# Kernel tuning notes

Hardware: AMD Instinct MI355X
Metric: run time of the kernel (lower is better)

The kernel has to match this reference:

```python
import jax, jax.numpy as jnp
import numpy as np
from jax import lax

D = 30   # embedding_dim (hardcoded in repo)
Q = 30   # question length
N = 4000 # number of sentences in doc
S = 100  # tokens per sentence
K = 5    # k_for_maxpool
SLOPE = 0.1  # LeakyReLU negative slope


def setup_inputs() -> dict:
    key = jax.random.key(0)
    ks = jax.random.split(key, 20)
    rn = lambda k, sh: jax.random.normal(k, sh, dtype=jnp.float32)
    ru = lambda k, sh: jax.random.uniform(k, sh, dtype=jnp.float32)
    return {
        "doc_sents_embeds": rn(ks[0], (N, S, D)),
        "sents_gaf": ru(ks[1], (N, 3)),
        "question_embeds": rn(ks[2], (Q, D)),
        "q_idfs": ru(ks[3], (Q, 1)),
        "doc_gaf": ru(ks[4], (4,)),
        "conv1_w": rn(ks[5], (D, D, 3)) * 0.1,
        "conv1_b": rn(ks[6], (D,)) * 0.1,
        "conv2_w": rn(ks[7], (D, D, 3)) * 0.1,
        "conv2_b": rn(ks[8], (D,)) * 0.1,
        "qw_W": rn(ks[9], (1, D + 1)) * 0.1,
        "qw_b": rn(ks[10], (1,)) * 0.1,
        "lq1_W": rn(ks[11], (8, 6)) * 0.1,
        "lq1_b": rn(ks[12], (8,)) * 0.1,
        "lq2_W": rn(ks[13], (1, 8)) * 0.1,
        "lq2_b": rn(ks[14], (1,)) * 0.1,
        "so_W": rn(ks[15], (1, 4)) * 0.1,
        "so_b": rn(ks[16], (1,)) * 0.1,
        "fl_W": rn(ks[17], (1, 5)) * 0.1,
        "fl_b": rn(ks[18], (1,)) * 0.1,
    }


def _leaky(x):
    return jnp.where(x >= 0, x, SLOPE * x)


def _conv_block(x, w, b):
    # x: [B, L, D]. torch Conv1d(D, D, 3, padding=2) then slice [1:L+1]
    # is exactly a 'same' conv with padding 1 on each side; then residual add.
    y = lax.conv_general_dilated(x.transpose(0, 2, 1), w, (1,), [(1, 1)],
                                 dimension_numbers=("NCH", "OIH", "NCH"))
    y = _leaky(y + b[None, :, None])
    return y.transpose(0, 2, 1) + x


def _cos_sim(A, B):
    # A: [Q, D], B: [N, S, D] -> [N, Q, S] (num/den as in torch my_cosine_sim)
    num = jnp.einsum("qd,nsd->nqs", A, B)
    den = jnp.linalg.norm(A, axis=-1)[None, :, None] * jnp.linalg.norm(B, axis=-1)[:, None, :]
    return num / den


def _pool(sim):
    # sort-based k-max pooling -> [max, avg_of_top_k]; sim: [N, Q, S] -> [N, Q, 2]
    vals = lax.top_k(sim, K)[0]  # descending
    return jnp.stack([vals[..., 0], vals.mean(-1)], axis=-1)


def reference(doc_sents_embeds, sents_gaf, question_embeds, q_idfs, doc_gaf,
              conv1_w, conv1_b, conv2_w, conv2_b, qw_W, qw_b,
              lq1_W, lq1_b, lq2_W, lq2_b, so_W, so_b, fl_W, fl_b):
    # question context (two residual trigram convs)
    q_conv = _conv_block(question_embeds[None], conv1_w, conv1_b)
    q_conv = _conv_block(q_conv, conv2_w, conv2_b)[0]          # [Q, D]
    # question term weights
    qw_in = jnp.concatenate([q_conv, q_idfs], axis=-1)          # [Q, D+1]
    q_weights = jax.nn.softmax((qw_in @ qw_W.T + qw_b)[:, 0])   # [Q]
    # sentence context convs (batched over all sentences)
    conv_res = _conv_block(doc_sents_embeds, conv1_w, conv1_b)
    conv_res = _conv_block(conv_res, conv2_w, conv2_b)          # [N, S, D]
    # similarity matrices
    sim_insens = _cos_sim(question_embeds, doc_sents_embeds)    # [N, Q, S]
    sim_oh = (sim_insens > 1.0 - 1e-3).astype(sim_insens.dtype)
    sim_sens = _cos_sim(q_conv, conv_res)
    # k-max pooling and per-q tiny MLP attention
    feats = jnp.concatenate([_pool(sim_oh), _pool(sim_insens), _pool(sim_sens)], axis=-1)  # [N, Q, 6]
    lo = _leaky(feats @ lq1_W.T + lq1_b) @ lq2_W.T + lq2_b      # [N, Q, 1]
    lo = lo[..., 0] * q_weights[None, :]
    sent_emit = lo.sum(-1) / Q                                  # [N]
    # per-sentence output layer
    sent_feats = jnp.concatenate([sents_gaf, sent_emit[:, None]], axis=-1)  # [N, 4]
    sent_scores = jax.nn.sigmoid((sent_feats @ so_W.T + so_b)[:, 0])        # [N]
    # doc-level score
    doc_rep = jnp.concatenate([jnp.max(sent_scores)[None], doc_gaf])        # [5]
    final = doc_rep @ fl_W.T + fl_b                                          # [1]
    return final, sent_scores
```

## Files before the change

### kernel.cpp

```cpp
#include <hip/hip_runtime.h>
#include <hip/hip_bf16.h>

#define SLOPE 0.1f

#define OFF_QW    1816
#define OFF_QNI   1846
#define OFF_QNS   1876
#define OFF_QNN   1906
#define OFF_B1    4606
#define OFF_B2    7336
#define OFF_LQ1W  7366
#define OFF_LQ1B  7414
#define OFF_LQ2W  7422
#define OFF_LQ2B  7430
#define OFF_SOW   7431
#define OFF_SOB   7435
#define OFF_FLW   7436
#define OFF_FLB   7441
#define U16_QEA   16384
#define U16_QCA   17408
#define U16_WB1   18432
#define U16_WB2   21504

typedef __attribute__((ext_vector_type(8))) __bf16 bf16x8;
typedef __attribute__((ext_vector_type(4))) float f32x4;

union Frag { uint4 u4; uint u[4]; bf16x8 v; };

__device__ __forceinline__ float bf2f(ushort h) {
    union { uint u; float f; } c; c.u = ((uint)h) << 16; return c.f;
}
__device__ __forceinline__ ushort f2bf(float f) {
    union { float f; uint u; } c; c.f = f;
    uint u = c.u;
    return (ushort)((u + 0x7FFFu + ((u >> 16) & 1u)) >> 16);
}
__device__ __forceinline__ float ldx(const void* p, long i, int bf) {
    if (bf) return bf2f(((const ushort*)p)[i]);
    return ((const float*)p)[i];
}
#define CE(x, y) { float _hi = fmaxf(x, y), _lo = fminf(x, y); x = _hi; y = _lo; }

__device__ __forceinline__ void sort4d(float& a, float& b, float& c, float& d) {
    CE(a, b); CE(c, d); CE(a, c); CE(b, d); CE(b, c);
}
__device__ __forceinline__ void merge44_5(const float* a, const float* b, float* t) {
    t[0] = fmaxf(a[0], b[0]);
    t[1] = fmaxf(fminf(a[0], b[0]), fmaxf(a[1], b[1]));
    t[2] = fmaxf(fmaxf(fminf(a[0], b[1]), fminf(a[1], b[0])), fmaxf(a[2], b[2]));
    t[3] = fmaxf(fmaxf(fminf(a[0], b[2]), fminf(a[1], b[1])),
                 fmaxf(fminf(a[2], b[0]), fmaxf(a[3], b[3])));
    t[4] = fmaxf(fmaxf(fminf(a[0], b[3]), fminf(a[1], b[2])),
                 fmaxf(fminf(a[2], b[1]), fminf(a[3], b[0])));
}
__device__ __forceinline__ void merge54_5(const float* a, const float* b, float* t) {
    t[0] = fmaxf(a[0], b[0]);
    t[1] = fmaxf(fminf(a[0], b[0]), fmaxf(a[1], b[1]));
    t[2] = fmaxf(fmaxf(fminf(a[0], b[1]), fminf(a[1], b[0])), fmaxf(a[2], b[2]));
    t[3] = fmaxf(fmaxf(fminf(a[0], b[2]), fminf(a[1], b[1])),
                 fmaxf(fminf(a[2], b[0]), fmaxf(a[3], b[3])));
    t[4] = fmaxf(fmaxf(fmaxf(fminf(a[0], b[3]), fminf(a[1], b[2])),
                       fmaxf(fminf(a[2], b[1]), fminf(a[3], b[0]))), a[4]);
}
__device__ __forceinline__ void merge55_5(const float* a, const float* b, float* t) {
    t[0] = fmaxf(a[0], b[0]);
    t[1] = fmaxf(fminf(a[0], b[0]), fmaxf(a[1], b[1]));
    t[2] = fmaxf(fmaxf(fminf(a[0], b[1]), fminf(a[1], b[0])), fmaxf(a[2], b[2]));
    t[3] = fmaxf(fmaxf(fminf(a[0], b[2]), fminf(a[1], b[1])),
                 fmaxf(fminf(a[2], b[0]), fmaxf(a[3], b[3])));
    t[4] = fmaxf(fmaxf(fmaxf(fminf(a[0], b[3]), fminf(a[1], b[2])),
                       fmaxf(fminf(a[2], b[1]), fminf(a[3], b[0]))),
                 fmaxf(a[4], b[4]));
}

__device__ __forceinline__ int detect_bf(const void* doc_in, int tid, int* scnt) {
    if (tid == 0) *scnt = 0;
    __syncthreads();
    const ushort* p = (const ushort*)doc_in;
    int local = 0;
    for (int i = tid; i < 4096; i += 256) {
        unsigned e = (p[i] >> 7) & 0xFFu;
        if (e != 0u && (e < 100u || e > 134u)) local++;
    }
    atomicAdd(scnt, local);
    __syncthreads();
    return (*scnt > 200) ? 0 : 1;
}

__global__ __launch_bounds__(256) void k_prep(
        const void* doc_in,
        const void* qe_in, const void* qidf_in,
        const void* w1_in, const void* b1_in,
        const void* w2_in, const void* b2_in,
        const void* qwW_in, const void* qwb_in,
        const void* lq1W_in, const void* lq1b_in,
        const void* lq2W_in, const void* lq2b_in,
        const void* soW_in, const void* sob_in,
        const void* flW_in, const void* flb_in,
        float* ws) {
    const int tid = threadIdx.x;
    const int blk = blockIdx.x;
    __shared__ float QE[900], T1[900], QC[900], W[2700], IDF[32], LG[32];
    __shared__ int scnt;

    const int bf = detect_bf(doc_in, tid, &scnt);
    ushort* wsu = (ushort*)ws;

    if (blk == 1) {
        if (tid == 0) { ((int*)ws)[0] = bf; }
        if (tid < 30) ws[OFF_B1 + tid] = ldx(b1_in, tid, bf);
        if (tid < 48) ws[OFF_LQ1W + tid] = ldx(lq1W_in, tid, bf);
        if (tid < 8)  { ws[OFF_LQ1B + tid] = ldx(lq1b_in, tid, bf);
                        ws[OFF_LQ2W + tid] = ldx(lq2W_in, tid, bf); }
        if (tid < 4)  ws[OFF_SOW + tid] = ldx(soW_in, tid, bf);
        if (tid < 5)  ws[OFF_FLW + tid] = ldx(flW_in, tid, bf);
        if (tid == 1) { ws[OFF_LQ2B] = ldx(lq2b_in, 0, bf);
                        ws[OFF_SOB]  = ldx(sob_in, 0, bf);
                        ws[OFF_FLB]  = ldx(flb_in, 0, bf); }
        for (int i = tid; i < 3072; i += 256) {
            int o = i / 96, kk = i % 96;
            float v1 = 0.f;
            if (o < 30 && kk < 90) {
                int ii = kk % 30, k = kk / 30;
                v1 = ldx(w1_in, (long)o*90 + ii*3 + k, bf);
            }
            wsu[U16_WB1 + i] = f2bf(v1);
        }
        return;
    }
    if (blk == 2) {
        if (tid < 30) ws[OFF_B2 + tid] = ldx(b2_in, tid, bf);
        for (int i = tid; i < 3072; i += 256) {
            int o = i / 96, kk = i % 96;
            float v2 = 0.f;
            if (o < 30 && kk < 90) {
                int ii = kk % 30, k = kk / 30;
                v2 = ldx(w2_in, (long)o*90 + ii*3 + k, bf);
            }
            wsu[U16_WB2 + i] = f2bf(v2);
        }
        return;
    }

    if (tid == 0) { ((int*)ws)[0] = bf; }

    for (int i = tid; i < 900; i += 256) QE[i] = ldx(qe_in, i, bf);
    if (tid < 30) IDF[tid] = ldx(qidf_in, tid, bf);
    for (int i = tid; i < 2700; i += 256) W[i] = ldx(w1_in, i, bf);
    __syncthreads();

    for (int idx = tid; idx < 900; idx += 256) {
        int s = idx / 30, o = idx % 30;
        float acc = ldx(b1_in, o, bf);
        for (int k = 0; k < 3; ++k) {
            int t = s + k - 1;
            if (t < 0 || t >= 30) continue;
            for (int i = 0; i < 30; ++i) acc += QE[t*30 + i] * W[o*90 + i*3 + k];
        }
        acc = acc >= 0.f ? acc : SLOPE * acc;
        T1[idx] = acc + QE[idx];
    }
    __syncthreads();
    for (int i = tid; i < 2700; i += 256) W[i] = ldx(w2_in, i, bf);
    __syncthreads();
    for (int idx = tid; idx < 900; idx += 256) {
        int s = idx / 30, o = idx % 30;
        float acc = ldx(b2_in, o, bf);
        for (int k = 0; k < 3; ++k) {
            int t = s + k - 1;
            if (t < 0 || t >= 30) continue;
            for (int i = 0; i < 30; ++i) acc += T1[t*30 + i] * W[o*90 + i*3 + k];
        }
        acc = acc >= 0.f ? acc : SLOPE * acc;
        QC[idx] = acc + T1[idx];
    }
    __syncthreads();

    if (tid < 30) {
        float s1 = 0.f, s2 = 0.f;
        for (int d = 0; d < 30; ++d) {
            float a = QE[tid*30 + d]; s1 += a*a;
            float b = QC[tid*30 + d]; s2 += b*b;
        }
        float n1 = sqrtf(s1);
        ws[OFF_QNN + tid] = n1;
        ws[OFF_QNI + tid] = 1.0f / n1;
        ws[OFF_QNS + tid] = 1.0f / sqrtf(s2);
        float z = ldx(qwb_in, 0, bf);
        for (int d = 0; d < 30; ++d) z += QC[tid*30 + d] * ldx(qwW_in, d, bf);
        z += IDF[tid] * ldx(qwW_in, 30, bf);
        LG[tid] = z;
    }
    __syncthreads();
    if (tid == 0) {
        float m = -1e30f;
        for (int q = 0; q < 30; ++q) m = fmaxf(m, LG[q]);
        float sum = 0.f, e[30];
        for (int q = 0; q < 30; ++q) { e[q] = expf(LG[q] - m); sum += e[q]; }
        for (int q = 0; q < 30; ++q) ws[OFF_QW + q] = e[q] / sum;
    }
    for (int i = tid; i < 1024; i += 256) {
        int q = i >> 5, d = i & 31;
        float ve = (q < 30 && d < 30) ? QE[q*30 + d] : 0.f;
        float vc = (q < 30 && d < 30) ? QC[q*30 + d] : 0.f;
        wsu[U16_QEA + i] = f2bf(ve);
        wsu[U16_QCA + i] = f2bf(vc);
    }
}

__global__ __launch_bounds__(128, 4) void k_main(const void* doc_in, const void* gaf_in,
                                                 void* out, float* ws) {
    const int n = blockIdx.x;
    const int tid = threadIdx.x;
    const int bf = ((const int*)ws)[0];
    const int lane = tid & 63;
    const int wid = tid >> 6;
    const int l15 = lane & 15;
    const int quad = lane >> 4;

    __shared__ uint XA32[1546];
    __shared__ uint XB32[1546];
    __shared__ __align__(16) float INVX[112];
    __shared__ float FE[30][6];
    __shared__ float IQI[32], IQS[32], QNN[32], BI1[32], BI2[32];

    ushort* XAu = (ushort*)XA32;
    const ushort* wsu = (const ushort*)ws;
    const uint4* qeA = (const uint4*)(wsu + U16_QEA);
    const uint4* qcA = (const uint4*)(wsu + U16_QCA);
    const uint4* wb1 = (const uint4*)(wsu + U16_WB1);
    const uint4* wb2 = (const uint4*)(wsu + U16_WB2);

    float ga0 = ldx(gaf_in, (long)n*3 + 0, bf);
    float ga1 = ldx(gaf_in, (long)n*3 + 1, bf);
    float ga2 = ldx(gaf_in, (long)n*3 + 2, bf);

    for (int i = tid; i < 46; i += 128) {
        int j = (i < 15) ? i : (1500 + i);
        XA32[j] = 0u; XB32[j] = 0u;
    }
    if (tid >= 100 && tid < 112) INVX[tid] = 0.f;
    if (bf) {
        const uint* g = (const uint*)((const ushort*)doc_in + (size_t)n * 3000);
        for (int i = tid; i < 1500; i += 128) XA32[15 + i] = g[i];
    } else {
        const float* p = (const float*)doc_in + (size_t)n * 3000;
        for (int i = tid; i < 3000; i += 128) XAu[30 + i] = f2bf(p[i]);
    }
    if (tid < 32) {
        IQI[tid] = ws[OFF_QNI + tid];
        IQS[tid] = ws[OFF_QNS + tid];
        QNN[tid] = ws[OFF_QNN + tid];
        BI1[tid] = ws[OFF_B1 + tid];
        BI2[tid] = ws[OFF_B2 + tid];
    }
    __syncthreads();

    if (tid < 100) {
        const uint* r = XA32 + (tid + 1) * 15;
        float s = 0.f;
        #pragma unroll
        for (int i = 0; i < 15; ++i) {
            uint u = r[i];
            float lo = __uint_as_float(u << 16);
            float hi = __uint_as_float(u & 0xFFFF0000u);
            s += lo * lo + hi * hi;
        }
        INVX[tid] = 1.f / sqrtf(s);
    }
    __syncthreads();

    auto sim_pool = [&](const uint4* qa, const float* IQ, int fbase, bool do_oh) {
        const int q = wid * 16 + l15;
        Frag b;
        b.u4 = qa[q * 4 + quad];
        f32x4 acc[7];
        #pragma unroll
        for (int mt = 0; mt < 7; ++mt) {
            int m = mt * 16 + l15;
            Frag a;
            if (m < 100) {
                int base = (m + 1) * 15 + quad * 4;
                a.u[0] = XA32[base];     a.u[1] = XA32[base + 1];
                a.u[2] = XA32[base + 2]; a.u[3] = XA32[base + 3];
            } else { a.u[0] = a.u[1] = a.u[2] = a.u[3] = 0u; }
            f32x4 z = {0.f, 0.f, 0.f, 0.f};
            acc[mt] = __builtin_amdgcn_mfma_f32_16x16x32_bf16(a.v, b.v, z, 0, 0, 0);
        }
        const float4* INVX4 = (const float4*)INVX;
        float thr = 0.999f * QNN[q];
        float iq  = (q < 30) ? IQ[q] : 0.f;
        float g[7][4];
        int cnt = 0;
        #pragma unroll
        for (int mt = 0; mt < 7; ++mt) {
            float4 ix = INVX4[mt * 4 + quad];
            float ixa[4] = {ix.x, ix.y, ix.z, ix.w};
            #pragma unroll
            for (int r = 0; r < 4; ++r) {
                float u = acc[mt][r] * ixa[r];
                if (mt == 6 && (quad * 4 + r) >= 4) u = -1e30f;
                g[mt][r] = u;
                if (do_oh) cnt += (u > thr) ? 1 : 0;
            }
        }
        #pragma unroll
        for (int mt = 0; mt < 7; ++mt) sort4d(g[mt][0], g[mt][1], g[mt][2], g[mt][3]);
        float p0[5], p1[5], p2[5], q0[5], q1[5], t[5];
        merge44_5(g[0], g[1], p0);
        merge44_5(g[2], g[3], p1);
        merge44_5(g[4], g[5], p2);
        merge55_5(p0, p1, q0);
        merge54_5(p2, g[6], q1);
        merge55_5(q0, q1, t);
        #pragma unroll
        for (int d = 16; d < 64; d <<= 1) {
            float pp[5];
            pp[0] = __shfl_xor(t[0], d); pp[1] = __shfl_xor(t[1], d);
            pp[2] = __shfl_xor(t[2], d); pp[3] = __shfl_xor(t[3], d);
            pp[4] = __shfl_xor(t[4], d);
            if (do_oh) cnt += __shfl_xor(cnt, d);
            float tn[5];
            merge55_5(t, pp, tn);
            t[0] = tn[0]; t[1] = tn[1]; t[2] = tn[2]; t[3] = tn[3]; t[4] = tn[4];
        }
        if (quad == 0 && q < 30) {
            if (do_oh) {
                FE[q][0] = cnt > 0 ? 1.f : 0.f;
                FE[q][1] = (float)(cnt > 5 ? 5 : cnt) * 0.2f;
            }
            FE[q][fbase]     = t[0] * iq;
            FE[q][fbase + 1] = (t[0] + t[1] + t[2] + t[3] + t[4]) * 0.2f * iq;
        }
    };

    auto conv_mt = [&](const uint* src32, uint* dst32, const uint4* wb,
                       const float* bias, int mt, int nt0, int nt1) {
        const ushort* srcU = (const ushort*)src32;
        ushort* dstU = (ushort*)dst32;
        int sa = mt * 16 + l15;
        Frag a[3];
        #pragma unroll
        for (int k = 0; k < 3; ++k) {
            if (sa < 100) {
                int base = sa * 15 + k * 16 + quad * 4;
                a[k].u[0] = src32[base];     a[k].u[1] = src32[base + 1];
                a[k].u[2] = src32[base + 2]; a[k].u[3] = src32[base + 3];
            } else { a[k].u[0] = a[k].u[1] = a[k].u[2] = a[k].u[3] = 0u; }
        }
        for (int nt = nt0; nt <= nt1; ++nt) {
            f32x4 acc = {0.f, 0.f, 0.f, 0.f};
            #pragma unroll
            for (int k = 0; k < 3; ++k) {
                Frag b;
                b.u4 = wb[(nt * 16 + l15) * 12 + k * 4 + quad];
                acc = __builtin_amdgcn_mfma_f32_16x16x32_bf16(a[k].v, b.v, acc, 0, 0, 0);
            }
            int o = nt * 16 + l15;
            if (o < 30) {
                float bo = bias[o];
                #pragma unroll
                for (int r = 0; r < 4; ++r) {
                    int s = mt * 16 + quad * 4 + r;
                    if (s < 100) {
                        float v = acc[r] + bo;
                        v = v >= 0.f ? v : SLOPE * v;
                        v += bf2f(srcU[(s + 1) * 30 + o]);
                        dstU[(s + 1) * 30 + o] = f2bf(v);
                    }
                }
            }
        }
    };

    sim_pool(qeA, IQI, 2, true);
    conv_mt(XA32, XB32, wb1, BI1, wid,     0, 1);
    conv_mt(XA32, XB32, wb1, BI1, wid + 2, 0, 1);
    conv_mt(XA32, XB32, wb1, BI1, wid + 4, 0, 1);
    conv_mt(XA32, XB32, wb1, BI1, 6,       wid, wid);
    __syncthreads();

    conv_mt(XB32, XA32, wb2, BI2, wid,     0, 1);
    conv_mt(XB32, XA32, wb2, BI2, wid + 2, 0, 1);
    conv_mt(XB32, XA32, wb2, BI2, wid + 4, 0, 1);
    conv_mt(XB32, XA32, wb2, BI2, 6,       wid, wid);
    __syncthreads();

    if (tid < 100) {
        const uint* r = XA32 + (tid + 1) * 15;
        float s = 0.f;
        #pragma unroll
        for (int i = 0; i < 15; ++i) {
            uint u = r[i];
            float lo = __uint_as_float(u << 16);
            float hi = __uint_as_float(u & 0xFFFF0000u);
            s += lo * lo + hi * hi;
        }
        INVX[tid] = 1.f / sqrtf(s);
    }
    __syncthreads();

    sim_pool(qcA, IQS, 4, false);
    __syncthreads();

    if (wid == 0) {
        float val = 0.f;
        if (lane < 30) {
            float lo = ws[OFF_LQ2B];
            #pragma unroll
            for (int j = 0; j < 8; ++j) {
                float h = ws[OFF_LQ1B + j];
                #pragma unroll
                for (int f = 0; f < 6; ++f) h += FE[lane][f] * ws[OFF_LQ1W + j*6 + f];
                h = h >= 0.f ? h : SLOPE * h;
                lo += h * ws[OFF_LQ2W + j];
            }
            val = lo * ws[OFF_QW + lane];
        }
        for (int d = 32; d >= 1; d >>= 1) val += __shfl_xor(val, d);
        if (lane == 0) {
            float emit = val * (1.f / 30.f);
            float z = ws[OFF_SOB];
            z += ga0 * ws[OFF_SOW + 0];
            z += ga1 * ws[OFF_SOW + 1];
            z += ga2 * ws[OFF_SOW + 2];
            z += emit * ws[OFF_SOW + 3];
            float sc = 1.f / (1.f + expf(-z));
            if (bf) ((__hip_bfloat16*)out)[1 + n] = __float2bfloat16(sc);
            else    ((float*)out)[1 + n] = sc;
        }
    }
}

__global__ __launch_bounds__(256) void k_final(const void* docgaf_in, void* out, const float* ws) {
    const int tid = threadIdx.x;
    const int bf = ((const int*)ws)[0];
    __shared__ float red[256];
    float m = -1e30f;
    for (int i = tid; i < 4000; i += 256) {
        float v = bf ? __bfloat162float(((const __hip_bfloat16*)out)[1 + i])
                     : ((const float*)out)[1 + i];
        m = fmaxf(m, v);
    }
    red[tid] = m;
    __syncthreads();
    for (int off = 128; off > 0; off >>= 1) {
        if (tid < off) red[tid] = fmaxf(red[tid], red[tid + off]);
        __syncthreads();
    }
    if (tid == 0) {
        float f = ws[OFF_FLB] + red[0] * ws[OFF_FLW + 0];
        for (int i = 0; i < 4; ++i) f += ldx(docgaf_in, i, bf) * ws[OFF_FLW + 1 + i];
        if (bf) ((__hip_bfloat16*)out)[0] = __float2bfloat16(f);
        else    ((float*)out)[0] = f;
    }
}

extern "C" void kernel_launch(void* const* d_in, const int* in_sizes, int n_in,
                              void* d_out, int out_size, void* d_ws, size_t ws_size,
                              hipStream_t stream) {
    float* ws = (float*)d_ws;
    k_prep<<<3, 256, 0, stream>>>(d_in[0], d_in[2], d_in[3], d_in[5], d_in[6], d_in[7], d_in[8],
                                  d_in[9], d_in[10], d_in[11], d_in[12], d_in[13], d_in[14],
                                  d_in[15], d_in[16], d_in[17], d_in[18], ws);
    k_main<<<4000, 128, 0, stream>>>(d_in[0], d_in[1], d_out, ws);
    k_final<<<1, 256, 0, stream>>>(d_in[4], d_out, ws);
}
```

Measured before the change: 176.9 us.

## Process one sentence per wavefront, removing block-level barriers and shared feature buffer

The main kernel now runs each sentence in its own 64-lane wavefront, two sentences per 128-thread block, so the __syncthreads between conv, norm and pooling stages go away. Each wave computes all 32 query columns with two MFMA accumulator sets and keeps the pooled features in registers, then does the MLP and a 16-lane shuffle reduction itself. The bf16 doc load now uses 16-byte vector copies into a 16-word-aligned buffer, and prep zero-pads entries 30-31 of the per-query and bias arrays. In exchange each wave does twice the work serially, register pressure rises (launch bounds lowered to 3 blocks), and shared memory per block doubles.

```diff
diff --git a/kernel.cpp b/kernel.cpp
--- a/kernel.cpp
+++ b/kernel.cpp
@@ -109,6 +109,7 @@
     if (blk == 1) {
         if (tid == 0) { ((int*)ws)[0] = bf; }
         if (tid < 30) ws[OFF_B1 + tid] = ldx(b1_in, tid, bf);
+        if (tid >= 30 && tid < 32) { ws[OFF_B1 + tid] = 0.f; ws[OFF_B2 + tid] = 0.f; }
         if (tid < 48) ws[OFF_LQ1W + tid] = ldx(lq1W_in, tid, bf);
         if (tid < 8)  { ws[OFF_LQ1B + tid] = ldx(lq1b_in, tid, bf);
                         ws[OFF_LQ2W + tid] = ldx(lq2W_in, tid, bf); }
@@ -143,6 +144,10 @@
     }
 
     if (tid == 0) { ((int*)ws)[0] = bf; }
+    if (tid >= 30 && tid < 32) {
+        ws[OFF_QW + tid] = 0.f; ws[OFF_QNI + tid] = 0.f;
+        ws[OFF_QNS + tid] = 0.f; ws[OFF_QNN + tid] = 0.f;
+    }
 
     for (int i = tid; i < 900; i += 256) QE[i] = ldx(qe_in, i, bf);
     if (tid < 30) IDF[tid] = ldx(qidf_in, tid, bf);
@@ -208,165 +213,188 @@
     }
 }
 
-__global__ __launch_bounds__(128, 4) void k_main(const void* doc_in, const void* gaf_in,
+__global__ __launch_bounds__(128, 3) void k_main(const void* doc_in, const void* gaf_in,
                                                  void* out, float* ws) {
-    const int n = blockIdx.x;
     const int tid = threadIdx.x;
-    const int bf = ((const int*)ws)[0];
+    const int wid = tid >> 6;
     const int lane = tid & 63;
-    const int wid = tid >> 6;
     const int l15 = lane & 15;
     const int quad = lane >> 4;
-
-    __shared__ uint XA32[1546];
-    __shared__ uint XB32[1546];
-    __shared__ __align__(16) float INVX[112];
-    __shared__ float FE[30][6];
-    __shared__ float IQI[32], IQS[32], QNN[32], BI1[32], BI2[32];
-
-    ushort* XAu = (ushort*)XA32;
+    const int sent = blockIdx.x * 2 + wid;
+    const int bf = ((const int*)ws)[0];
+
+    __shared__ __align__(16) uint XAbuf[2][1546];
+    __shared__ __align__(16) uint XBbuf[2][1546];
+    __shared__ __align__(16) float INVXbuf[2][112];
+    __shared__ float IQI[32], IQS[32], QNN[32], BI1[32], BI2[32], QWs[32];
+
+    uint* XA = XAbuf[wid];
+    uint* XB = XBbuf[wid];
+    float* IX = INVXbuf[wid];
+    ushort* XAu = (ushort*)XA;
+
     const ushort* wsu = (const ushort*)ws;
     const uint4* qeA = (const uint4*)(wsu + U16_QEA);
     const uint4* qcA = (const uint4*)(wsu + U16_QCA);
     const uint4* wb1 = (const uint4*)(wsu + U16_WB1);
     const uint4* wb2 = (const uint4*)(wsu + U16_WB2);
 
-    float ga0 = ldx(gaf_in, (long)n*3 + 0, bf);
-    float ga1 = ldx(gaf_in, (long)n*3 + 1, bf);
-    float ga2 = ldx(gaf_in, (long)n*3 + 2, bf);
-
-    for (int i = tid; i < 46; i += 128) {
-        int j = (i < 15) ? i : (1500 + i);
-        XA32[j] = 0u; XB32[j] = 0u;
-    }
-    if (tid >= 100 && tid < 112) INVX[tid] = 0.f;
+    float ga0 = ldx(gaf_in, (long)sent*3 + 0, bf);
+    float ga1 = ldx(gaf_in, (long)sent*3 + 1, bf);
+    float ga2 = ldx(gaf_in, (long)sent*3 + 2, bf);
+
+    if (lane < 32) {
+        IQI[lane] = ws[OFF_QNI + lane];
+        IQS[lane] = ws[OFF_QNS + lane];
+        QNN[lane] = ws[OFF_QNN + lane];
+        BI1[lane] = ws[OFF_B1 + lane];
+        BI2[lane] = ws[OFF_B2 + lane];
+        QWs[lane] = ws[OFF_QW + lane];
+    }
+
+    if (lane < 46) {
+        int j = (lane < 16) ? lane : (1500 + lane);
+        XA[j] = 0u; XB[j] = 0u;
+    }
     if (bf) {
-        const uint* g = (const uint*)((const ushort*)doc_in + (size_t)n * 3000);
-        for (int i = tid; i < 1500; i += 128) XA32[15 + i] = g[i];
+        const uint4* g = (const uint4*)((const ushort*)doc_in + (size_t)sent * 3000);
+        uint4* dst = (uint4*)(XA + 16);
+        for (int i = lane; i < 375; i += 64) dst[i] = g[i];
     } else {
-        const float* p = (const float*)doc_in + (size_t)n * 3000;
-        for (int i = tid; i < 3000; i += 128) XAu[30 + i] = f2bf(p[i]);
-    }
-    if (tid < 32) {
-        IQI[tid] = ws[OFF_QNI + tid];
-        IQS[tid] = ws[OFF_QNS + tid];
-        QNN[tid] = ws[OFF_QNN + tid];
-        BI1[tid] = ws[OFF_B1 + tid];
-        BI2[tid] = ws[OFF_B2 + tid];
-    }
-    __syncthreads();
-
-    if (tid < 100) {
-        const uint* r = XA32 + (tid + 1) * 15;
-        float s = 0.f;
-        #pragma unroll
-        for (int i = 0; i < 15; ++i) {
-            uint u = r[i];
-            float lo = __uint_as_float(u << 16);
-            float hi = __uint_as_float(u & 0xFFFF0000u);
-            s += lo * lo + hi * hi;
-        }
-        INVX[tid] = 1.f / sqrtf(s);
-    }
-    __syncthreads();
-
+        const float* p = (const float*)doc_in + (size_t)sent * 3000;
+        for (int i = lane; i < 3000; i += 64) XAu[32 + i] = f2bf(p[i]);
+    }
+
+    auto norms = [&](const uint* src) {
+        #pragma unroll
+        for (int pass = 0; pass < 2; ++pass) {
+            int s = lane + pass * 64;
+            if (s < 100) {
+                const uint* r = src + 16 + s * 15;
+                float sum = 0.f;
+                #pragma unroll
+                for (int i = 0; i < 15; ++i) {
+                    uint u = r[i];
+                    float lo = __uint_as_float(u << 16);
+                    float hi = __uint_as_float(u & 0xFFFF0000u);
+                    sum += lo * lo + hi * hi;
+                }
+                IX[s] = 1.f / sqrtf(sum);
+            }
+        }
+        if (lane >= 36 && lane < 48) IX[lane + 64] = 0.f;
+    };
+    norms(XA);
+
+    float fe[2][6];
     auto sim_pool = [&](const uint4* qa, const float* IQ, int fbase, bool do_oh) {
-        const int q = wid * 16 + l15;
-        Frag b;
-        b.u4 = qa[q * 4 + quad];
-        f32x4 acc[7];
+        Frag b0, b1;
+        b0.u4 = qa[l15 * 4 + quad];
+        b1.u4 = qa[(16 + l15) * 4 + quad];
+        f32x4 acc0[7], acc1[7];
         #pragma unroll
         for (int mt = 0; mt < 7; ++mt) {
             int m = mt * 16 + l15;
             Frag a;
             if (m < 100) {
-                int base = (m + 1) * 15 + quad * 4;
-                a.u[0] = XA32[base];     a.u[1] = XA32[base + 1];
-                a.u[2] = XA32[base + 2]; a.u[3] = XA32[base + 3];
+                int base = 16 + m * 15 + quad * 4;
+                a.u[0] = XA[base];     a.u[1] = XA[base + 1];
+                a.u[2] = XA[base + 2]; a.u[3] = XA[base + 3];
             } else { a.u[0] = a.u[1] = a.u[2] = a.u[3] = 0u; }
             f32x4 z = {0.f, 0.f, 0.f, 0.f};
-            acc[mt] = __builtin_amdgcn_mfma_f32_16x16x32_bf16(a.v, b.v, z, 0, 0, 0);
-        }
-        const float4* INVX4 = (const float4*)INVX;
-        float thr = 0.999f * QNN[q];
-        float iq  = (q < 30) ? IQ[q] : 0.f;
-        float g[7][4];
-        int cnt = 0;
+            acc0[mt] = __builtin_amdgcn_mfma_f32_16x16x32_bf16(a.v, b0.v, z, 0, 0, 0);
+            acc1[mt] = __builtin_amdgcn_mfma_f32_16x16x32_bf16(a.v, b1.v, z, 0, 0, 0);
+        }
+        float ixa[7][4];
+        const float4* IX4 = (const float4*)IX;
         #pragma unroll
         for (int mt = 0; mt < 7; ++mt) {
-            float4 ix = INVX4[mt * 4 + quad];
-            float ixa[4] = {ix.x, ix.y, ix.z, ix.w};
-            #pragma unroll
-            for (int r = 0; r < 4; ++r) {
-                float u = acc[mt][r] * ixa[r];
-                if (mt == 6 && (quad * 4 + r) >= 4) u = -1e30f;
-                g[mt][r] = u;
-                if (do_oh) cnt += (u > thr) ? 1 : 0;
-            }
-        }
-        #pragma unroll
-        for (int mt = 0; mt < 7; ++mt) sort4d(g[mt][0], g[mt][1], g[mt][2], g[mt][3]);
-        float p0[5], p1[5], p2[5], q0[5], q1[5], t[5];
-        merge44_5(g[0], g[1], p0);
-        merge44_5(g[2], g[3], p1);
-        merge44_5(g[4], g[5], p2);
-        merge55_5(p0, p1, q0);
-        merge54_5(p2, g[6], q1);
-        merge55_5(q0, q1, t);
-        #pragma unroll
-        for (int d = 16; d < 64; d <<= 1) {
-            float pp[5];
-            pp[0] = __shfl_xor(t[0], d); pp[1] = __shfl_xor(t[1], d);
-            pp[2] = __shfl_xor(t[2], d); pp[3] = __shfl_xor(t[3], d);
-            pp[4] = __shfl_xor(t[4], d);
-            if (do_oh) cnt += __shfl_xor(cnt, d);
-            float tn[5];
-            merge55_5(t, pp, tn);
-            t[0] = tn[0]; t[1] = tn[1]; t[2] = tn[2]; t[3] = tn[3]; t[4] = tn[4];
-        }
-        if (quad == 0 && q < 30) {
-            if (do_oh) {
-                FE[q][0] = cnt > 0 ? 1.f : 0.f;
-                FE[q][1] = (float)(cnt > 5 ? 5 : cnt) * 0.2f;
-            }
-            FE[q][fbase]     = t[0] * iq;
-            FE[q][fbase + 1] = (t[0] + t[1] + t[2] + t[3] + t[4]) * 0.2f * iq;
-        }
-    };
-
-    auto conv_mt = [&](const uint* src32, uint* dst32, const uint4* wb,
-                       const float* bias, int mt, int nt0, int nt1) {
-        const ushort* srcU = (const ushort*)src32;
-        ushort* dstU = (ushort*)dst32;
-        int sa = mt * 16 + l15;
-        Frag a[3];
-        #pragma unroll
-        for (int k = 0; k < 3; ++k) {
-            if (sa < 100) {
-                int base = sa * 15 + k * 16 + quad * 4;
-                a[k].u[0] = src32[base];     a[k].u[1] = src32[base + 1];
-                a[k].u[2] = src32[base + 2]; a[k].u[3] = src32[base + 3];
-            } else { a[k].u[0] = a[k].u[1] = a[k].u[2] = a[k].u[3] = 0u; }
-        }
-        for (int nt = nt0; nt <= nt1; ++nt) {
-            f32x4 acc = {0.f, 0.f, 0.f, 0.f};
-            #pragma unroll
-            for (int k = 0; k < 3; ++k) {
-                Frag b;
-                b.u4 = wb[(nt * 16 + l15) * 12 + k * 4 + quad];
-                acc = __builtin_amdgcn_mfma_f32_16x16x32_bf16(a[k].v, b.v, acc, 0, 0, 0);
-            }
-            int o = nt * 16 + l15;
-            if (o < 30) {
-                float bo = bias[o];
+            float4 v4 = IX4[mt * 4 + quad];
+            ixa[mt][0] = v4.x; ixa[mt][1] = v4.y; ixa[mt][2] = v4.z; ixa[mt][3] = v4.w;
+        }
+        #pragma unroll
+        for (int t = 0; t < 2; ++t) {
+            const f32x4* acc = t ? acc1 : acc0;
+            int q = t * 16 + l15;
+            float thr = 0.999f * QNN[q];
+            float iq  = IQ[q];
+            float g[7][4];
+            int cnt = 0;
+            #pragma unroll
+            for (int mt = 0; mt < 7; ++mt) {
                 #pragma unroll
                 for (int r = 0; r < 4; ++r) {
-                    int s = mt * 16 + quad * 4 + r;
-                    if (s < 100) {
-                        float v = acc[r] + bo;
-                        v = v >= 0.f ? v : SLOPE * v;
-                        v += bf2f(srcU[(s + 1) * 30 + o]);
-                        dstU[(s + 1) * 30 + o] = f2bf(v);
+                    float u = acc[mt][r] * ixa[mt][r];
+                    if (mt == 6 && (quad * 4 + r) >= 4) u = -1e30f;
+                    g[mt][r] = u;
+                    if (do_oh) cnt += (u > thr) ? 1 : 0;
+                }
+            }
+            #pragma unroll
+            for (int mt = 0; mt < 7; ++mt) sort4d(g[mt][0], g[mt][1], g[mt][2], g[mt][3]);
+            float p0[5], p1[5], p2[5], q0[5], q1[5], tt[5];
+            merge44_5(g[0], g[1], p0);
+            merge44_5(g[2], g[3], p1);
+            merge44_5(g[4], g[5], p2);
+            merge55_5(p0, p1, q0);
+            merge54_5(p2, g[6], q1);
+            merge55_5(q0, q1, tt);
+            #pragma unroll
+            for (int d = 16; d < 64; d <<= 1) {
+                float pp[5];
+                pp[0] = __shfl_xor(tt[0], d); pp[1] = __shfl_xor(tt[1], d);
+                pp[2] = __shfl_xor(tt[2], d); pp[3] = __shfl_xor(tt[3], d);
+                pp[4] = __shfl_xor(tt[4], d);
+                if (do_oh) cnt += __shfl_xor(cnt, d);
+                float tn[5];
+                merge55_5(tt, pp, tn);
+                tt[0] = tn[0]; tt[1] = tn[1]; tt[2] = tn[2]; tt[3] = tn[3]; tt[4] = tn[4];
+            }
+            if (do_oh) {
+                fe[t][0] = cnt > 0 ? 1.f : 0.f;
+                fe[t][1] = (float)(cnt > 5 ? 5 : cnt) * 0.2f;
+            }
+            fe[t][fbase]     = tt[0] * iq;
+            fe[t][fbase + 1] = (tt[0] + tt[1] + tt[2] + tt[3] + tt[4]) * 0.2f * iq;
+        }
+    };
+
+    auto conv = [&](const uint* src, uint* dst, const uint4* wb, const float* bias) {
+        const ushort* srcU = (const ushort*)src;
+        ushort* dstU = (ushort*)dst;
+        #pragma unroll
+        for (int mt = 0; mt < 7; ++mt) {
+            int sa = mt * 16 + l15;
+            Frag a[3];
+            #pragma unroll
+            for (int k = 0; k < 3; ++k) {
+                if (sa < 100) {
+                    int base = 16 + (sa - 1) * 15 + k * 16 + quad * 4;
+                    a[k].u[0] = src[base];     a[k].u[1] = src[base + 1];
+                    a[k].u[2] = src[base + 2]; a[k].u[3] = src[base + 3];
+                } else { a[k].u[0] = a[k].u[1] = a[k].u[2] = a[k].u[3] = 0u; }
+            }
+            #pragma unroll
+            for (int nt = 0; nt < 2; ++nt) {
+                f32x4 acc = {0.f, 0.f, 0.f, 0.f};
+                #pragma unroll
+                for (int k = 0; k < 3; ++k) {
+                    Frag b;
+                    b.u4 = wb[(nt * 16 + l15) * 12 + k * 4 + quad];
+                    acc = __builtin_amdgcn_mfma_f32_16x16x32_bf16(a[k].v, b.v, acc, 0, 0, 0);
+                }
+                int o = nt * 16 + l15;
+                if (o < 30) {
+                    float bo = bias[o];
+                    #pragma unroll
+                    for (int r = 0; r < 4; ++r) {
+                        int s = mt * 16 + quad * 4 + r;
+                        if (s < 100) {
+                            float v = acc[r] + bo;
+                            v = fmaxf(v, SLOPE * v);
+                            v += bf2f(srcU[32 + s * 30 + o]);
+                            dstU[32 + s * 30 + o] = f2bf(v);
+                        }
                     }
                 }
             }
@@ -374,61 +402,36 @@
     };
 
     sim_pool(qeA, IQI, 2, true);
-    conv_mt(XA32, XB32, wb1, BI1, wid,     0, 1);
-    conv_mt(XA32, XB32, wb1, BI1, wid + 2, 0, 1);
-    conv_mt(XA32, XB32, wb1, BI1, wid + 4, 0, 1);
-    conv_mt(XA32, XB32, wb1, BI1, 6,       wid, wid);
-    __syncthreads();
-
-    conv_mt(XB32, XA32, wb2, BI2, wid,     0, 1);
-    conv_mt(XB32, XA32, wb2, BI2, wid + 2, 0, 1);
-    conv_mt(XB32, XA32, wb2, BI2, wid + 4, 0, 1);
-    conv_mt(XB32, XA32, wb2, BI2, 6,       wid, wid);
-    __syncthreads();
-
-    if (tid < 100) {
-        const uint* r = XA32 + (tid + 1) * 15;
-        float s = 0.f;
-        #pragma unroll
-        for (int i = 0; i < 15; ++i) {
-            uint u = r[i];
-            float lo = __uint_as_float(u << 16);
-            float hi = __uint_as_float(u & 0xFFFF0000u);
-            s += lo * lo + hi * hi;
-        }
-        INVX[tid] = 1.f / sqrtf(s);
-    }
-    __syncthreads();
-
+    conv(XA, XB, wb1, BI1);
+    conv(XB, XA, wb2, BI2);
+    norms(XA);
     sim_pool(qcA, IQS, 4, false);
-    __syncthreads();
-
-    if (wid == 0) {
-        float val = 0.f;
-        if (lane < 30) {
-            float lo = ws[OFF_LQ2B];
-            #pragma unroll
-            for (int j = 0; j < 8; ++j) {
-                float h = ws[OFF_LQ1B + j];
-                #pragma unroll
-                for (int f = 0; f < 6; ++f) h += FE[lane][f] * ws[OFF_LQ1W + j*6 + f];
-                h = h >= 0.f ? h : SLOPE * h;
-                lo += h * ws[OFF_LQ2W + j];
-            }
-            val = lo * ws[OFF_QW + lane];
-        }
-        for (int d = 32; d >= 1; d >>= 1) val += __shfl_xor(val, d);
-        if (lane == 0) {
-            float emit = val * (1.f / 30.f);
-            float z = ws[OFF_SOB];
-            z += ga0 * ws[OFF_SOW + 0];
-            z += ga1 * ws[OFF_SOW + 1];
-            z += ga2 * ws[OFF_SOW + 2];
-            z += emit * ws[OFF_SOW + 3];
-            float sc = 1.f / (1.f + expf(-z));
-            if (bf) ((__hip_bfloat16*)out)[1 + n] = __float2bfloat16(sc);
-            else    ((float*)out)[1 + n] = sc;
-        }
+
+    auto mlp = [&](const float* f) {
+        float lo = ws[OFF_LQ2B];
+        #pragma unroll
+        for (int j = 0; j < 8; ++j) {
+            float h = ws[OFF_LQ1B + j];
+            #pragma unroll
+            for (int c = 0; c < 6; ++c) h += f[c] * ws[OFF_LQ1W + j*6 + c];
+            h = fmaxf(h, SLOPE * h);
+            lo += h * ws[OFF_LQ2W + j];
+        }
+        return lo;
+    };
+    float val = mlp(fe[0]) * QWs[l15] + mlp(fe[1]) * QWs[16 + l15];
+    #pragma unroll
+    for (int d = 1; d < 16; d <<= 1) val += __shfl_xor(val, d);
+    if (lane == 0) {
+        float emit = val * (1.f / 30.f);
+        float z = ws[OFF_SOB];
+        z += ga0 * ws[OFF_SOW + 0];
+        z += ga1 * ws[OFF_SOW + 1];
+        z += ga2 * ws[OFF_SOW + 2];
+        z += emit * ws[OFF_SOW + 3];
+        float sc = 1.f / (1.f + expf(-z));
+        if (bf) ((__hip_bfloat16*)out)[1 + sent] = __float2bfloat16(sc);
+        else    ((float*)out)[1 + sent] = sc;
     }
 }
 
@@ -463,6 +466,6 @@
     k_prep<<<3, 256, 0, stream>>>(d_in[0], d_in[2], d_in[3], d_in[5], d_in[6], d_in[7], d_in[8],
                                   d_in[9], d_in[10], d_in[11], d_in[12], d_in[13], d_in[14],
                                   d_in[15], d_in[16], d_in[17], d_in[18], ws);
-    k_main<<<4000, 128, 0, stream>>>(d_in[0], d_in[1], d_out, ws);
+    k_main<<<2000, 128, 0, stream>>>(d_in[0], d_in[1], d_out, ws);
     k_final<<<1, 256, 0, stream>>>(d_in[4], d_out, ws);
 }
```

New measurement: 209.6 us. 18.5% more time.
